# Performance work log

Measured on AMD Instinct MI355X. Metric: run time of the kernel, lower is better.

The kernel has to match this reference:

```python
import math
import jax, jax.numpy as jnp
import numpy as np

B, S, D, H, REL_V = 2, 2048, 1024, 16, 64
HD = D // H
EPS = 1e-5


def _layernorm(x, w, b):
    # torch-style: std with Bessel correction (unbiased), divide by (std + eps)
    u = x.mean(-1, keepdims=True)
    xc = x - u
    s = jnp.sqrt((xc * xc).sum(-1, keepdims=True) / (x.shape[-1] - 1))
    return w * (xc / (s + EPS)) + b


def _gelu(x):
    return 0.5 * x * (1 + jnp.tanh(math.sqrt(2 / math.pi) * (x + 0.044715 * x ** 3)))


def setup_inputs() -> dict:
    key = jax.random.key(0)
    ks = jax.random.split(key, 6)
    wscale = 0.02
    return {
        "x": jax.random.normal(ks[0], (B, S, D), jnp.float32),
        "rel": jax.random.randint(ks[1], (B, S, S), 0, REL_V, jnp.int32),
        "ln1_w": jnp.ones((D,), jnp.float32),
        "ln1_b": jnp.zeros((D,), jnp.float32),
        "Wqkv": jax.random.normal(ks[2], (D, 3 * D), jnp.float32) * wscale,
        "bqkv": jnp.zeros((3 * D,), jnp.float32),
        "Wo": jax.random.normal(ks[3], (D, D), jnp.float32) * wscale,
        "bo": jnp.zeros((D,), jnp.float32),
        "rel_emb": jax.random.normal(ks[4], (REL_V, H), jnp.float32) * wscale,
        "ln2_w": jnp.ones((D,), jnp.float32),
        "ln2_b": jnp.zeros((D,), jnp.float32),
        "Wfc": jax.random.normal(ks[5], (D, 4 * D), jnp.float32) * wscale,
        "bfc": jnp.zeros((4 * D,), jnp.float32),
        "Wp": jax.random.normal(jax.random.fold_in(key, 7), (4 * D, D), jnp.float32) * wscale,
        "bp": jnp.zeros((D,), jnp.float32),
    }


def reference(x, rel, ln1_w, ln1_b, Wqkv, bqkv, Wo, bo, rel_emb,
              ln2_w, ln2_b, Wfc, bfc, Wp, bp):
    h = _layernorm(x, ln1_w, ln1_b)
    qkv = h @ Wqkv + bqkv  # [B,S,3D]
    q, k, v = jnp.split(qkv, 3, axis=-1)
    q = q.reshape(B, S, H, HD).transpose(0, 2, 1, 3)  # [B,H,S,HD]
    k = k.reshape(B, S, H, HD).transpose(0, 2, 1, 3)
    v = v.reshape(B, S, H, HD).transpose(0, 2, 1, 3)

    w = jnp.einsum('bhqd,bhkd->bhqk', q, k) / math.sqrt(HD)  # scale=True
    mask = jnp.tril(jnp.ones((S, S), w.dtype))  # causal tril buffer
    w = w * mask - 1e10 * (1 - mask)
    # faithful to original: rel bias multiplies masked logits (zeroing masked -1e10)
    relw = rel_emb[rel]                    # [B,S,S,H]
    relw = relw.transpose(0, 3, 1, 2)      # [B,H,S,S]
    w = w * (relw * mask)
    p = jax.nn.softmax(w, axis=-1)
    a = jnp.einsum('bhqk,bhkd->bhqd', p, v)       # [B,H,S,HD]
    a = a.transpose(0, 2, 1, 3).reshape(B, S, D)  # merge heads
    a = a @ Wo + bo

    x = x + a
    m = _gelu(_layernorm(x, ln2_w, ln2_b) @ Wfc + bfc) @ Wp + bp
    return x + m
```

## Files before the change

kernel.cpp:

```cpp
#include <hip/hip_runtime.h>
#include <hip/hip_bf16.h>
#include <math.h>

using bf16 = __hip_bfloat16;
typedef __bf16 bf16x8 __attribute__((ext_vector_type(8)));
typedef float f32x4 __attribute__((ext_vector_type(4)));

#define SEQ 2048
#define DIM 1024
#define NH 16
#define HDIM 64
#define BATCH 2

__device__ __forceinline__ void load_lds16(const bf16* g, bf16* l) {
  __builtin_amdgcn_global_load_lds((__attribute__((address_space(1))) void*)g,
                                   (__attribute__((address_space(3))) void*)l, 16, 0, 0);
}

__global__ __launch_bounds__(256) void transpose_k(const float* __restrict__ in,
                                                   bf16* __restrict__ out, int R, int C) {
  __shared__ float tile[32][33];
  int c0 = blockIdx.x * 32, r0 = blockIdx.y * 32;
  int tx = threadIdx.x, ty = threadIdx.y;
#pragma unroll
  for (int j = 0; j < 4; ++j)
    tile[ty + 8 * j][tx] = in[(size_t)(r0 + ty + 8 * j) * C + c0 + tx];
  __syncthreads();
#pragma unroll
  for (int j = 0; j < 4; ++j)
    out[(size_t)(c0 + ty + 8 * j) * R + r0 + tx] = __float2bfloat16(tile[tx][ty + 8 * j]);
}

__global__ __launch_bounds__(256) void ln_k(const float* __restrict__ x,
                                            const float* __restrict__ w,
                                            const float* __restrict__ bb,
                                            bf16* __restrict__ out) {
  int row = blockIdx.x, tid = threadIdx.x;
  int wid = tid >> 6, lane = tid & 63;
  const float* xr = x + (size_t)row * DIM;
  float4 vv = *(const float4*)&xr[tid * 4];
  float v[4] = {vv.x, vv.y, vv.z, vv.w};
  float s = v[0] + v[1] + v[2] + v[3];
#pragma unroll
  for (int m = 1; m < 64; m <<= 1) s += __shfl_xor(s, m, 64);
  __shared__ float red[8];
  if (lane == 0) red[wid] = s;
  __syncthreads();
  float mean = (red[0] + red[1] + red[2] + red[3]) * (1.f / DIM);
  float q = 0.f;
#pragma unroll
  for (int j = 0; j < 4; ++j) {
    v[j] -= mean;
    q += v[j] * v[j];
  }
#pragma unroll
  for (int m = 1; m < 64; m <<= 1) q += __shfl_xor(q, m, 64);
  if (lane == 0) red[4 + wid] = q;
  __syncthreads();
  float ssq = red[4] + red[5] + red[6] + red[7];
  float sd = sqrtf(ssq / (float)(DIM - 1));
  float inv = 1.f / (sd + 1e-5f);
  float4 wv = *(const float4*)&w[tid * 4];
  float4 bv4 = *(const float4*)&bb[tid * 4];
  float wl[4] = {wv.x, wv.y, wv.z, wv.w};
  float bl[4] = {bv4.x, bv4.y, bv4.z, bv4.w};
  unsigned short pk[4];
#pragma unroll
  for (int j = 0; j < 4; ++j)
    pk[j] = __bfloat16_as_ushort(__float2bfloat16(wl[j] * (v[j] * inv) + bl[j]));
  *(uint2*)&out[(size_t)row * DIM + tid * 4] = *(uint2*)pk;
}

__global__ __launch_bounds__(512) void gemm256_k(
    const bf16* __restrict__ A, const bf16* __restrict__ Bt, const float* __restrict__ bias,
    int N, int K, int mode, bf16* __restrict__ o0, bf16* __restrict__ o1,
    bf16* __restrict__ o2) {
  __shared__ bf16 LDSb[65536];
  int tid = threadIdx.x;
  int wid = tid >> 6, lane = tid & 63, quad = lane >> 4, l15 = lane & 15;
  int wm = wid >> 2, wn = wid & 3;
  int m0 = blockIdx.y * 256, n0 = blockIdx.x * 256;
  int grow = lane >> 2;
  int gslot = (lane & 3) ^ ((lane >> 3) & 3);
  const int nt = K >> 6;

  float bv[4];
#pragma unroll
  for (int nf = 0; nf < 4; ++nf) bv[nf] = bias[n0 + wn * 64 + nf * 16 + l15];

  auto stageA = [&](int tile, int ks) {
    int bd = tile & 1;
#pragma unroll
    for (int it = 0; it < 2; ++it) {
      int c = wid * 2 + it;
      load_lds16(A + (size_t)(m0 + c * 16 + grow) * K + tile * 64 + ks * 32 + gslot * 8,
                 &LDSb[bd * 32768 + ks * 8192 + c * 512]);
    }
  };
  auto stageB = [&](int tile, int ks) {
    int bd = tile & 1;
#pragma unroll
    for (int it = 0; it < 2; ++it) {
      int c = wid * 2 + it;
      load_lds16(Bt + (size_t)(n0 + c * 16 + grow) * K + tile * 64 + ks * 32 + gslot * 8,
                 &LDSb[bd * 32768 + 16384 + ks * 8192 + c * 512]);
    }
  };

  f32x4 acc[8][4] = {};
  bf16x8 bq[4];

  stageA(0, 0); stageB(0, 0);
  stageA(0, 1); stageB(0, 1);
  stageA(1, 0); stageB(1, 0);
  asm volatile("s_waitcnt vmcnt(8)" ::: "memory");
  __builtin_amdgcn_sched_barrier(0);
  __builtin_amdgcn_s_barrier();
  __builtin_amdgcn_sched_barrier(0);

#define PHASE(BD, KS, MH, LOADB, STAGE_STMT, WAIT_STMT)                                      \
  {                                                                                          \
    bf16x8 af[4];                                                                            \
    _Pragma("unroll") for (int j = 0; j < 4; ++j) {                                          \
      int r = wm * 128 + (MH) * 64 + j * 16 + l15;                                           \
      af[j] = *(const bf16x8*)&LDSb[(BD) * 32768 + (KS) * 8192 + (r >> 4) * 512 +            \
                                    (r & 15) * 32 + ((quad ^ ((r >> 1) & 3)) << 3)];         \
    }                                                                                        \
    if (LOADB) {                                                                             \
      _Pragma("unroll") for (int n = 0; n < 4; ++n) {                                        \
        int r = wn * 64 + n * 16 + l15;                                                      \
        bq[n] = *(const bf16x8*)&LDSb[(BD) * 32768 + 16384 + (KS) * 8192 + (r >> 4) * 512 +  \
                                      (r & 15) * 32 + ((quad ^ ((r >> 1) & 3)) << 3)];       \
      }                                                                                      \
    }                                                                                        \
    STAGE_STMT;                                                                              \
    __builtin_amdgcn_sched_barrier(0);                                                       \
    __builtin_amdgcn_s_barrier();                                                            \
    __builtin_amdgcn_sched_barrier(0);                                                       \
    __builtin_amdgcn_s_setprio(1);                                                           \
    _Pragma("unroll") for (int j = 0; j < 4; ++j)                                            \
        _Pragma("unroll") for (int n = 0; n < 4; ++n)                                        \
            acc[(MH) * 4 + j][n] = __builtin_amdgcn_mfma_f32_16x16x32_bf16(                  \
                af[j], bq[n], acc[(MH) * 4 + j][n], 0, 0, 0);                                \
    __builtin_amdgcn_s_setprio(0);                                                           \
    WAIT_STMT;                                                                               \
    __builtin_amdgcn_sched_barrier(0);                                                       \
    __builtin_amdgcn_s_barrier();                                                            \
    __builtin_amdgcn_sched_barrier(0);                                                       \
  }

  for (int t = 0; t < nt; ++t) {
    int bd = t & 1;
    PHASE(bd, 0, 0, 1, { if (t + 1 < nt) stageA(t + 1, 1); }, {});
    PHASE(bd, 0, 1, 0, { if (t + 1 < nt) stageB(t + 1, 1); }, {
      if (t + 1 < nt) asm volatile("s_waitcnt vmcnt(8)" ::: "memory");
      else            asm volatile("s_waitcnt vmcnt(0)" ::: "memory");
    });
    PHASE(bd, 1, 0, 1, { if (t + 2 < nt) stageA(t + 2, 0); }, {});
    PHASE(bd, 1, 1, 0, { if (t + 2 < nt) stageB(t + 2, 0); }, {
      if (t + 2 < nt)      asm volatile("s_waitcnt vmcnt(8)" ::: "memory");
      else if (t + 1 < nt) asm volatile("s_waitcnt vmcnt(4)" ::: "memory");
    });
  }
#undef PHASE

#pragma unroll
  for (int mf = 0; mf < 8; ++mf) {
#pragma unroll
    for (int nf = 0; nf < 4; ++nf) {
      int col = n0 + wn * 64 + nf * 16 + l15;
      int row_base = m0 + wm * 128 + mf * 16 + quad * 4;
      if (mode == 0) {
        int which = col >> 10, d = col & 1023, hh = d >> 6, dd = d & 63;
        int b = row_base >> 11, s2 = row_base & 2047;
        if (which == 2) {
          unsigned short pk[4];
#pragma unroll
          for (int r = 0; r < 4; ++r)
            pk[r] = __bfloat16_as_ushort(__float2bfloat16(acc[mf][nf][r] + bv[nf]));
          *(uint2*)&o2[(((size_t)b * NH + hh) * HDIM + dd) * SEQ + s2] = *(uint2*)pk;
        } else {
          bf16* dst = which == 0 ? o0 : o1;
#pragma unroll
          for (int r = 0; r < 4; ++r)
            dst[(((size_t)b * NH + hh) * SEQ + s2 + r) * HDIM + dd] =
                __float2bfloat16(acc[mf][nf][r] + bv[nf]);
        }
      } else {
#pragma unroll
        for (int r = 0; r < 4; ++r) {
          float t2 = acc[mf][nf][r] + bv[nf];
          float u = 0.7978845608028654f * (t2 + 0.044715f * t2 * t2 * t2);
          float g = t2 / (1.f + __expf(-2.f * u));
          o0[(size_t)(row_base + r) * N + col] = __float2bfloat16(g);
        }
      }
    }
  }
}

template <int TM>
__global__ __launch_bounds__(256) void gemm_k(
    const bf16* __restrict__ A, const bf16* __restrict__ Bt, const float* __restrict__ bias,
    int M, int N, int K, int mode,
    const float* __restrict__ residf, float* __restrict__ x2out, const float* __restrict__ x2in,
    float* __restrict__ outf) {
  constexpr int MT = TM / 32;
  constexpr int ACH = TM / 8;
  __shared__ bf16 As[TM * 64];
  __shared__ bf16 Bs[128 * 64];
  int tid = threadIdx.x;
  int wid = tid >> 6, lane = tid & 63, quad = lane >> 4, l15 = lane & 15;
  int wm = wid >> 1, wn = wid & 1;
  int m0 = blockIdx.y * TM, n0 = blockIdx.x * 128;
  int rsub = lane >> 3;
  int c8 = (lane & 7) ^ rsub;
  f32x4 acc[MT][4] = {};

  for (int k0 = 0; k0 < K; k0 += 64) {
    __syncthreads();
#pragma unroll
    for (int it = 0; it < ACH / 4; ++it) {
      int c = wid * (ACH / 4) + it;
      int row = c * 8 + rsub;
      load_lds16(A + (size_t)(m0 + row) * K + k0 + c8 * 8, &As[c * 512]);
    }
#pragma unroll
    for (int it = 0; it < 4; ++it) {
      int c = wid * 4 + it;
      int row = c * 8 + rsub;
      load_lds16(Bt + (size_t)(n0 + row) * K + k0 + c8 * 8, &Bs[c * 512]);
    }
    __syncthreads();
#pragma unroll
    for (int ks = 0; ks < 2; ++ks) {
      bf16x8 af[MT], bfr[4];
#pragma unroll
      for (int mt = 0; mt < MT; ++mt) {
        int r = wm * (MT * 16) + mt * 16 + l15;
        af[mt] = *(const bf16x8*)&As[r * 64 + ((ks * 4 + quad) ^ (r & 7)) * 8];
      }
#pragma unroll
      for (int nt2 = 0; nt2 < 4; ++nt2) {
        int r = wn * 64 + nt2 * 16 + l15;
        bfr[nt2] = *(const bf16x8*)&Bs[r * 64 + ((ks * 4 + quad) ^ (r & 7)) * 8];
      }
#pragma unroll
      for (int mt = 0; mt < MT; ++mt)
#pragma unroll
        for (int nt2 = 0; nt2 < 4; ++nt2)
          acc[mt][nt2] =
              __builtin_amdgcn_mfma_f32_16x16x32_bf16(af[mt], bfr[nt2], acc[mt][nt2], 0, 0, 0);
    }
  }

#pragma unroll
  for (int mt = 0; mt < MT; ++mt) {
#pragma unroll
    for (int nt = 0; nt < 4; ++nt) {
      int col = n0 + wn * 64 + nt * 16 + l15;
      float bvs = bias[col];
      int row_base = m0 + wm * (MT * 16) + mt * 16 + quad * 4;
#pragma unroll
      for (int r = 0; r < 4; ++r) {
        int row = row_base + r;
        float val = acc[mt][nt][r] + bvs;
        size_t i = (size_t)row * N + col;
        if (mode == 1) x2out[i] = residf[i] + val;
        else           outf[i] = x2in[i] + val;
      }
    }
  }
}

__global__ __launch_bounds__(256) void sufv_k(const bf16* __restrict__ vt,
                                              float* __restrict__ suf) {
  int row = blockIdx.x;
  const bf16* src = vt + (size_t)row * SEQ;
  float* dst = suf + (size_t)row * SEQ;
  int tid = threadIdx.x;
  float v[8];
  float s = 0.f;
#pragma unroll
  for (int j = 0; j < 8; ++j) {
    v[j] = __bfloat162float(src[tid * 8 + j]);
    s += v[j];
  }
  __shared__ float sc[256];
  sc[tid] = s;
  __syncthreads();
  for (int off = 1; off < 256; off <<= 1) {
    float add = (tid + off < 256) ? sc[tid + off] : 0.f;
    __syncthreads();
    sc[tid] += add;
    __syncthreads();
  }
  float run = (tid < 255) ? sc[tid + 1] : 0.f;
#pragma unroll
  for (int j = 7; j >= 0; --j) {
    dst[tid * 8 + j] = run;
    run += v[j];
  }
}

__device__ __forceinline__ int pswz(int row) { return (row & 7) ^ (((row >> 3) & 1) << 1); }

__global__ __launch_bounds__(256) void attn_k(const bf16* __restrict__ q,
                                              const bf16* __restrict__ k,
                                              const bf16* __restrict__ v,
                                              const int* __restrict__ rel,
                                              const float* __restrict__ rel_emb,
                                              const float* __restrict__ suf,
                                              bf16* __restrict__ out) {
  int h = blockIdx.x;
  int qt = (SEQ / 64 - 1) - blockIdx.y;
  int b = blockIdx.z;
  int tid = threadIdx.x;
  int wid = tid >> 6, lane = tid & 63, quad = lane >> 4, l15 = lane & 15;

  __shared__ __align__(16) char SM[40960];
  bf16* Kb = (bf16*)SM;
  bf16* Vb = (bf16*)(SM + 16384);
  bf16* Ps = (bf16*)(SM + 32768);
  float(*SufLds)[68] = (float(*)[68])SM;

  const size_t bh = (size_t)b * NH + h;
  const bf16* qb = q + (bh * SEQ + (size_t)qt * 64) * HDIM;
  const bf16* kb0 = k + bh * SEQ * HDIM;
  const bf16* vt0 = v + bh * (size_t)HDIM * SEQ;

  float rv = 0.125f * rel_emb[lane * NH + h];

  int rsub = lane >> 3;
  int c8 = (lane & 7) ^ rsub;

  bf16x8 aq[2];
#pragma unroll
  for (int ks = 0; ks < 2; ++ks)
    aq[ks] = *(const bf16x8*)(qb + (size_t)(wid * 16 + l15) * HDIM + ks * 32 + quad * 8);

#pragma unroll
  for (int it = 0; it < 2; ++it) {
    int c = wid * 2 + it;
    int row = c * 8 + rsub;
    load_lds16(kb0 + (size_t)row * HDIM + c8 * 8, &Kb[c * 512]);
    load_lds16(vt0 + (size_t)row * SEQ + c8 * 8, &Vb[c * 512]);
  }

  const int* relq = rel + (size_t)b * SEQ * SEQ + (size_t)qt * 64 * SEQ;
  const int* rp[4];
#pragma unroll
  for (int r = 0; r < 4; ++r) rp[r] = relq + (size_t)(wid * 16 + quad * 4 + r) * SEQ;

  int ridx[4][4];
#pragma unroll
  for (int nt = 0; nt < 4; ++nt)
#pragma unroll
    for (int r = 0; r < 4; ++r) ridx[nt][r] = rp[r][nt * 16 + l15];

  __syncthreads();

  const int q_base = qt * 64 + wid * 16 + quad * 4;
  const int prow_w = wid * 16 + quad * 4;
  const int prow_r = wid * 16 + l15;
  const int psw_r = pswz(prow_r);
  float l_part[4] = {0.f, 0.f, 0.f, 0.f};
  f32x4 o_acc[4] = {};

  for (int kt = 0; kt < qt; ++kt) {
    int cur = kt & 1;
    int ridx2[4][4];
    {
      bf16* Kd = Kb + (cur ^ 1) * 4096;
      bf16* Vd = Vb + (cur ^ 1) * 4096;
#pragma unroll
      for (int it = 0; it < 2; ++it) {
        int c = wid * 2 + it;
        int row = c * 8 + rsub;
        load_lds16(kb0 + (size_t)((kt + 1) * 64 + row) * HDIM + c8 * 8, &Kd[c * 512]);
        load_lds16(vt0 + (size_t)row * SEQ + (kt + 1) * 64 + c8 * 8, &Vd[c * 512]);
      }
#pragma unroll
      for (int nt = 0; nt < 4; ++nt)
#pragma unroll
        for (int r = 0; r < 4; ++r) ridx2[nt][r] = rp[r][(kt + 1) * 64 + nt * 16 + l15];
    }

    const bf16* Ksb = Kb + cur * 4096;
    const bf16* Vtb = Vb + cur * 4096;

    f32x4 sacc[4] = {};
    __builtin_amdgcn_s_setprio(1);
#pragma unroll
    for (int ks = 0; ks < 2; ++ks) {
#pragma unroll
      for (int nt = 0; nt < 4; ++nt) {
        bf16x8 bfr = *(const bf16x8*)&Ksb[(nt * 16 + l15) * 64 + ((ks * 4 + quad) ^ (l15 & 7)) * 8];
        sacc[nt] = __builtin_amdgcn_mfma_f32_16x16x32_bf16(aq[ks], bfr, sacc[nt], 0, 0, 0);
      }
    }
    __builtin_amdgcn_s_setprio(0);

#pragma unroll
    for (int nt = 0; nt < 4; ++nt) {
#pragma unroll
      for (int r = 0; r < 4; ++r) {
        float m = __shfl(rv, ridx[nt][r], 64);
        float p = __expf(sacc[nt][r] * m);
        l_part[r] += p;
        int row = prow_w + r;
        int sw = (nt * 2 + (l15 >> 3)) ^ pswz(row);
        Ps[row * 64 + sw * 8 + (l15 & 7)] = __float2bfloat16(p);
      }
    }

    __builtin_amdgcn_s_setprio(1);
#pragma unroll
    for (int ks = 0; ks < 2; ++ks) {
      bf16x8 af = *(const bf16x8*)&Ps[prow_r * 64 + ((ks * 4 + quad) ^ psw_r) * 8];
#pragma unroll
      for (int nt = 0; nt < 4; ++nt) {
        bf16x8 bfr = *(const bf16x8*)&Vtb[(nt * 16 + l15) * 64 + ((ks * 4 + quad) ^ (l15 & 7)) * 8];
        o_acc[nt] = __builtin_amdgcn_mfma_f32_16x16x32_bf16(af, bfr, o_acc[nt], 0, 0, 0);
      }
    }
    __builtin_amdgcn_s_setprio(0);

    __syncthreads();

#pragma unroll
    for (int nt = 0; nt < 4; ++nt)
#pragma unroll
      for (int r = 0; r < 4; ++r) ridx[nt][r] = ridx2[nt][r];
  }

  {
    int cur = qt & 1;
    const bf16* Ksb = Kb + cur * 4096;
    const bf16* Vtb = Vb + cur * 4096;

    f32x4 sacc[4] = {};
    __builtin_amdgcn_s_setprio(1);
#pragma unroll
    for (int ks = 0; ks < 2; ++ks) {
#pragma unroll
      for (int nt = 0; nt < 4; ++nt) {
        bf16x8 bfr = *(const bf16x8*)&Ksb[(nt * 16 + l15) * 64 + ((ks * 4 + quad) ^ (l15 & 7)) * 8];
        sacc[nt] = __builtin_amdgcn_mfma_f32_16x16x32_bf16(aq[ks], bfr, sacc[nt], 0, 0, 0);
      }
    }
    __builtin_amdgcn_s_setprio(0);

#pragma unroll
    for (int nt = 0; nt < 4; ++nt) {
#pragma unroll
      for (int r = 0; r < 4; ++r) {
        float m = __shfl(rv, ridx[nt][r], 64);
        float p = __expf(sacc[nt][r] * m);
        int k_abs = qt * 64 + nt * 16 + l15;
        if (k_abs > q_base + r) p = 0.f;
        l_part[r] += p;
        int row = prow_w + r;
        int sw = (nt * 2 + (l15 >> 3)) ^ pswz(row);
        Ps[row * 64 + sw * 8 + (l15 & 7)] = __float2bfloat16(p);
      }
    }

    __builtin_amdgcn_s_setprio(1);
#pragma unroll
    for (int ks = 0; ks < 2; ++ks) {
      bf16x8 af = *(const bf16x8*)&Ps[prow_r * 64 + ((ks * 4 + quad) ^ psw_r) * 8];
#pragma unroll
      for (int nt = 0; nt < 4; ++nt) {
        bf16x8 bfr = *(const bf16x8*)&Vtb[(nt * 16 + l15) * 64 + ((ks * 4 + quad) ^ (l15 & 7)) * 8];
        o_acc[nt] = __builtin_amdgcn_mfma_f32_16x16x32_bf16(af, bfr, o_acc[nt], 0, 0, 0);
      }
    }
    __builtin_amdgcn_s_setprio(0);

    __syncthreads();
  }

#pragma unroll
  for (int r = 0; r < 4; ++r)
#pragma unroll
    for (int m = 1; m < 16; m <<= 1) l_part[r] += __shfl_xor(l_part[r], m, 64);

  const float* sufb = suf + bh * (size_t)HDIM * SEQ + (size_t)qt * 64;
#pragma unroll
  for (int p = 0; p < 4; ++p) {
    int idx = p * 256 + tid;
    int d = idx >> 4, qq = idx & 15;
    *(float4*)&SufLds[d][qq * 4] = *(const float4*)(sufb + (size_t)d * SEQ + qq * 4);
  }
  __syncthreads();

#pragma unroll
  for (int nt = 0; nt < 4; ++nt) {
    int d = nt * 16 + l15;
#pragma unroll
    for (int r = 0; r < 4; ++r) {
      int row = q_base + r;
      int cnt = (SEQ - 1) - row;
      float l = l_part[r] + (float)cnt;
      int q_local = wid * 16 + quad * 4 + r;
      float ov = (o_acc[nt][r] + SufLds[d][q_local]) / l;
      out[((size_t)b * SEQ + row) * DIM + h * HDIM + d] = __float2bfloat16(ov);
    }
  }
}

extern "C" void kernel_launch(void* const* d_in, const int* in_sizes, int n_in,
                              void* d_out, int out_size, void* d_ws, size_t ws_size,
                              hipStream_t stream) {
  const float* x = (const float*)d_in[0];
  const int* rel = (const int*)d_in[1];
  const float* ln1w = (const float*)d_in[2];
  const float* ln1b = (const float*)d_in[3];
  const float* Wqkv = (const float*)d_in[4];
  const float* bqkv = (const float*)d_in[5];
  const float* Wo = (const float*)d_in[6];
  const float* bo = (const float*)d_in[7];
  const float* rel_emb = (const float*)d_in[8];
  const float* ln2w = (const float*)d_in[9];
  const float* ln2b = (const float*)d_in[10];
  const float* Wfc = (const float*)d_in[11];
  const float* bfc = (const float*)d_in[12];
  const float* Wp = (const float*)d_in[13];
  const float* bp = (const float*)d_in[14];
  float* outp = (float*)d_out;

  char* ws = (char*)d_ws;
  const size_t MB = 1u << 20;
  bf16* h = (bf16*)(ws + 0);
  bf16* qb = (bf16*)(ws + 8 * MB);
  bf16* kb = (bf16*)(ws + 16 * MB);
  bf16* vb = (bf16*)(ws + 24 * MB);
  float* x2 = (float*)(ws + 32 * MB);
  float* suf = (float*)(ws + 32 * MB);
  bf16* fcb = (bf16*)(ws + 48 * MB);
  bf16* wqkvT = (bf16*)(ws + 48 * MB);
  bf16* woT = (bf16*)(ws + 54 * MB);
  bf16* wfcT = (bf16*)(ws + 16 * MB);
  bf16* wpT = (bf16*)(ws + 24 * MB);

  dim3 tb(32, 8);
  transpose_k<<<dim3(3072 / 32, 1024 / 32), tb, 0, stream>>>(Wqkv, wqkvT, 1024, 3072);
  transpose_k<<<dim3(1024 / 32, 1024 / 32), tb, 0, stream>>>(Wo, woT, 1024, 1024);

  ln_k<<<BATCH * SEQ, 256, 0, stream>>>(x, ln1w, ln1b, h);

  gemm256_k<<<dim3(3072 / 256, 4096 / 256), 512, 0, stream>>>(
      h, wqkvT, bqkv, 3072, 1024, 0, qb, kb, vb);

  sufv_k<<<BATCH * NH * HDIM, 256, 0, stream>>>(vb, suf);

  attn_k<<<dim3(NH, SEQ / 64, BATCH), 256, 0, stream>>>(qb, kb, vb, rel, rel_emb, suf, h);

  gemm_k<64><<<dim3(1024 / 128, 4096 / 64), 256, 0, stream>>>(
      h, woT, bo, BATCH * SEQ, 1024, 1024, 1, x, x2, nullptr, nullptr);

  transpose_k<<<dim3(4096 / 32, 1024 / 32), tb, 0, stream>>>(Wfc, wfcT, 1024, 4096);
  transpose_k<<<dim3(1024 / 32, 4096 / 32), tb, 0, stream>>>(Wp, wpT, 4096, 1024);

  ln_k<<<BATCH * SEQ, 256, 0, stream>>>(x2, ln2w, ln2b, qb);

  gemm256_k<<<dim3(4096 / 256, 4096 / 256), 512, 0, stream>>>(
      qb, wfcT, bfc, 4096, 1024, 2, fcb, nullptr, nullptr);

  gemm_k<64><<<dim3(1024 / 128, 4096 / 64), 256, 0, stream>>>(
      fcb, wpT, bp, BATCH * SEQ, 1024, 4096, 3, nullptr, nullptr, x2, outp);
}
```

Before: 399.9 us.

## Pair complementary causal query tiles per block to balance attention work

The attention kernel now launches 512-thread blocks, where each block handles two query tiles: tile 31-y and tile y. This pairs long and short causal rows so every block does about the same number of K/V tiles. The two 4-wave groups share one set of K/V tiles loaded into LDS, and the group with the short tile sits idle on the later iterations. This removes the tail imbalance of the causal grid and halves the K/V reloads. The cost is idle waves in the short group, larger LDS per block and fewer blocks.

```diff
diff --git a/kernel.cpp b/kernel.cpp
--- a/kernel.cpp
+++ b/kernel.cpp
@@ -305,7 +305,7 @@
 
 __device__ __forceinline__ int pswz(int row) { return (row & 7) ^ (((row >> 3) & 1) << 1); }
 
-__global__ __launch_bounds__(256) void attn_k(const bf16* __restrict__ q,
+__global__ __launch_bounds__(512) void attn_k(const bf16* __restrict__ q,
                                               const bf16* __restrict__ k,
                                               const bf16* __restrict__ v,
                                               const int* __restrict__ rel,
@@ -313,21 +313,25 @@
                                               const float* __restrict__ suf,
                                               bf16* __restrict__ out) {
   int h = blockIdx.x;
-  int qt = (SEQ / 64 - 1) - blockIdx.y;
+  int y = blockIdx.y;
   int b = blockIdx.z;
   int tid = threadIdx.x;
   int wid = tid >> 6, lane = tid & 63, quad = lane >> 4, l15 = lane & 15;
-
-  __shared__ __align__(16) char SM[40960];
+  int g = wid >> 2;
+  int w4 = wid & 3;
+
+  __shared__ __align__(16) char SM[49152];
   bf16* Kb = (bf16*)SM;
   bf16* Vb = (bf16*)(SM + 16384);
   bf16* Ps = (bf16*)(SM + 32768);
-  float(*SufLds)[68] = (float(*)[68])SM;
+
+  const int qt_hi = 31 - y;
+  const int qtg = g ? y : qt_hi;
 
   const size_t bh = (size_t)b * NH + h;
-  const bf16* qb = q + (bh * SEQ + (size_t)qt * 64) * HDIM;
   const bf16* kb0 = k + bh * SEQ * HDIM;
   const bf16* vt0 = v + bh * (size_t)HDIM * SEQ;
+  const bf16* qb = q + (bh * SEQ + (size_t)qtg * 64) * HDIM;
 
   float rv = 0.125f * rel_emb[lane * NH + h];
 
@@ -337,20 +341,19 @@
   bf16x8 aq[2];
 #pragma unroll
   for (int ks = 0; ks < 2; ++ks)
-    aq[ks] = *(const bf16x8*)(qb + (size_t)(wid * 16 + l15) * HDIM + ks * 32 + quad * 8);
-
-#pragma unroll
-  for (int it = 0; it < 2; ++it) {
-    int c = wid * 2 + it;
+    aq[ks] = *(const bf16x8*)(qb + (size_t)(w4 * 16 + l15) * HDIM + ks * 32 + quad * 8);
+
+  {
+    int c = wid;
     int row = c * 8 + rsub;
     load_lds16(kb0 + (size_t)row * HDIM + c8 * 8, &Kb[c * 512]);
     load_lds16(vt0 + (size_t)row * SEQ + c8 * 8, &Vb[c * 512]);
   }
 
-  const int* relq = rel + (size_t)b * SEQ * SEQ + (size_t)qt * 64 * SEQ;
+  const int* relq = rel + (size_t)b * SEQ * SEQ + (size_t)qtg * 64 * SEQ;
   const int* rp[4];
 #pragma unroll
-  for (int r = 0; r < 4; ++r) rp[r] = relq + (size_t)(wid * 16 + quad * 4 + r) * SEQ;
+  for (int r = 0; r < 4; ++r) rp[r] = relq + (size_t)(w4 * 16 + quad * 4 + r) * SEQ;
 
   int ridx[4][4];
 #pragma unroll
@@ -360,125 +363,102 @@
 
   __syncthreads();
 
-  const int q_base = qt * 64 + wid * 16 + quad * 4;
-  const int prow_w = wid * 16 + quad * 4;
-  const int prow_r = wid * 16 + l15;
+  const int q_base = qtg * 64 + w4 * 16 + quad * 4;
+  const int prow_w = g * 64 + w4 * 16 + quad * 4;
+  const int prow_r = g * 64 + w4 * 16 + l15;
   const int psw_r = pswz(prow_r);
   float l_part[4] = {0.f, 0.f, 0.f, 0.f};
   f32x4 o_acc[4] = {};
 
-  for (int kt = 0; kt < qt; ++kt) {
+  for (int kt = 0; kt <= qt_hi; ++kt) {
     int cur = kt & 1;
-    int ridx2[4][4];
-    {
+
+    if (kt < qt_hi) {
       bf16* Kd = Kb + (cur ^ 1) * 4096;
       bf16* Vd = Vb + (cur ^ 1) * 4096;
-#pragma unroll
-      for (int it = 0; it < 2; ++it) {
-        int c = wid * 2 + it;
-        int row = c * 8 + rsub;
-        load_lds16(kb0 + (size_t)((kt + 1) * 64 + row) * HDIM + c8 * 8, &Kd[c * 512]);
-        load_lds16(vt0 + (size_t)row * SEQ + (kt + 1) * 64 + c8 * 8, &Vd[c * 512]);
-      }
+      int c = wid;
+      int row = c * 8 + rsub;
+      load_lds16(kb0 + (size_t)((kt + 1) * 64 + row) * HDIM + c8 * 8, &Kd[c * 512]);
+      load_lds16(vt0 + (size_t)row * SEQ + (kt + 1) * 64 + c8 * 8, &Vd[c * 512]);
+    }
+    int ridx2[4][4];
+    bool nxt_active = (kt < qt_hi) && (kt + 1 <= qtg);
+    if (nxt_active) {
 #pragma unroll
       for (int nt = 0; nt < 4; ++nt)
 #pragma unroll
         for (int r = 0; r < 4; ++r) ridx2[nt][r] = rp[r][(kt + 1) * 64 + nt * 16 + l15];
     }
 
-    const bf16* Ksb = Kb + cur * 4096;
-    const bf16* Vtb = Vb + cur * 4096;
-
-    f32x4 sacc[4] = {};
-    __builtin_amdgcn_s_setprio(1);
-#pragma unroll
-    for (int ks = 0; ks < 2; ++ks) {
-#pragma unroll
-      for (int nt = 0; nt < 4; ++nt) {
-        bf16x8 bfr = *(const bf16x8*)&Ksb[(nt * 16 + l15) * 64 + ((ks * 4 + quad) ^ (l15 & 7)) * 8];
-        sacc[nt] = __builtin_amdgcn_mfma_f32_16x16x32_bf16(aq[ks], bfr, sacc[nt], 0, 0, 0);
-      }
-    }
-    __builtin_amdgcn_s_setprio(0);
-
-#pragma unroll
-    for (int nt = 0; nt < 4; ++nt) {
-#pragma unroll
-      for (int r = 0; r < 4; ++r) {
-        float m = __shfl(rv, ridx[nt][r], 64);
-        float p = __expf(sacc[nt][r] * m);
-        l_part[r] += p;
-        int row = prow_w + r;
-        int sw = (nt * 2 + (l15 >> 3)) ^ pswz(row);
-        Ps[row * 64 + sw * 8 + (l15 & 7)] = __float2bfloat16(p);
-      }
-    }
-
-    __builtin_amdgcn_s_setprio(1);
-#pragma unroll
-    for (int ks = 0; ks < 2; ++ks) {
-      bf16x8 af = *(const bf16x8*)&Ps[prow_r * 64 + ((ks * 4 + quad) ^ psw_r) * 8];
-#pragma unroll
-      for (int nt = 0; nt < 4; ++nt) {
-        bf16x8 bfr = *(const bf16x8*)&Vtb[(nt * 16 + l15) * 64 + ((ks * 4 + quad) ^ (l15 & 7)) * 8];
-        o_acc[nt] = __builtin_amdgcn_mfma_f32_16x16x32_bf16(af, bfr, o_acc[nt], 0, 0, 0);
-      }
-    }
-    __builtin_amdgcn_s_setprio(0);
+    if (kt <= qtg) {
+      const bf16* Ksb = Kb + cur * 4096;
+      const bf16* Vtb = Vb + cur * 4096;
+
+      f32x4 sacc[4] = {};
+      __builtin_amdgcn_s_setprio(1);
+#pragma unroll
+      for (int ks = 0; ks < 2; ++ks) {
+#pragma unroll
+        for (int nt = 0; nt < 4; ++nt) {
+          bf16x8 bfr =
+              *(const bf16x8*)&Ksb[(nt * 16 + l15) * 64 + ((ks * 4 + quad) ^ (l15 & 7)) * 8];
+          sacc[nt] = __builtin_amdgcn_mfma_f32_16x16x32_bf16(aq[ks], bfr, sacc[nt], 0, 0, 0);
+        }
+      }
+      __builtin_amdgcn_s_setprio(0);
+
+      if (kt == qtg) {
+#pragma unroll
+        for (int nt = 0; nt < 4; ++nt) {
+#pragma unroll
+          for (int r = 0; r < 4; ++r) {
+            float m = __shfl(rv, ridx[nt][r], 64);
+            float p = __expf(sacc[nt][r] * m);
+            int k_abs = kt * 64 + nt * 16 + l15;
+            if (k_abs > q_base + r) p = 0.f;
+            l_part[r] += p;
+            int row = prow_w + r;
+            int sw = (nt * 2 + (l15 >> 3)) ^ pswz(row);
+            Ps[row * 64 + sw * 8 + (l15 & 7)] = __float2bfloat16(p);
+          }
+        }
+      } else {
+#pragma unroll
+        for (int nt = 0; nt < 4; ++nt) {
+#pragma unroll
+          for (int r = 0; r < 4; ++r) {
+            float m = __shfl(rv, ridx[nt][r], 64);
+            float p = __expf(sacc[nt][r] * m);
+            l_part[r] += p;
+            int row = prow_w + r;
+            int sw = (nt * 2 + (l15 >> 3)) ^ pswz(row);
+            Ps[row * 64 + sw * 8 + (l15 & 7)] = __float2bfloat16(p);
+          }
+        }
+      }
+
+      __builtin_amdgcn_s_setprio(1);
+#pragma unroll
+      for (int ks = 0; ks < 2; ++ks) {
+        bf16x8 af = *(const bf16x8*)&Ps[prow_r * 64 + ((ks * 4 + quad) ^ psw_r) * 8];
+#pragma unroll
+        for (int nt = 0; nt < 4; ++nt) {
+          bf16x8 bfr =
+              *(const bf16x8*)&Vtb[(nt * 16 + l15) * 64 + ((ks * 4 + quad) ^ (l15 & 7)) * 8];
+          o_acc[nt] = __builtin_amdgcn_mfma_f32_16x16x32_bf16(af, bfr, o_acc[nt], 0, 0, 0);
+        }
+      }
+      __builtin_amdgcn_s_setprio(0);
+    }
 
     __syncthreads();
 
-#pragma unroll
-    for (int nt = 0; nt < 4; ++nt)
-#pragma unroll
-      for (int r = 0; r < 4; ++r) ridx[nt][r] = ridx2[nt][r];
-  }
-
-  {
-    int cur = qt & 1;
-    const bf16* Ksb = Kb + cur * 4096;
-    const bf16* Vtb = Vb + cur * 4096;
-
-    f32x4 sacc[4] = {};
-    __builtin_amdgcn_s_setprio(1);
-#pragma unroll
-    for (int ks = 0; ks < 2; ++ks) {
-#pragma unroll
-      for (int nt = 0; nt < 4; ++nt) {
-        bf16x8 bfr = *(const bf16x8*)&Ksb[(nt * 16 + l15) * 64 + ((ks * 4 + quad) ^ (l15 & 7)) * 8];
-        sacc[nt] = __builtin_amdgcn_mfma_f32_16x16x32_bf16(aq[ks], bfr, sacc[nt], 0, 0, 0);
-      }
-    }
-    __builtin_amdgcn_s_setprio(0);
-
-#pragma unroll
-    for (int nt = 0; nt < 4; ++nt) {
-#pragma unroll
-      for (int r = 0; r < 4; ++r) {
-        float m = __shfl(rv, ridx[nt][r], 64);
-        float p = __expf(sacc[nt][r] * m);
-        int k_abs = qt * 64 + nt * 16 + l15;
-        if (k_abs > q_base + r) p = 0.f;
-        l_part[r] += p;
-        int row = prow_w + r;
-        int sw = (nt * 2 + (l15 >> 3)) ^ pswz(row);
-        Ps[row * 64 + sw * 8 + (l15 & 7)] = __float2bfloat16(p);
-      }
-    }
-
-    __builtin_amdgcn_s_setprio(1);
-#pragma unroll
-    for (int ks = 0; ks < 2; ++ks) {
-      bf16x8 af = *(const bf16x8*)&Ps[prow_r * 64 + ((ks * 4 + quad) ^ psw_r) * 8];
-#pragma unroll
-      for (int nt = 0; nt < 4; ++nt) {
-        bf16x8 bfr = *(const bf16x8*)&Vtb[(nt * 16 + l15) * 64 + ((ks * 4 + quad) ^ (l15 & 7)) * 8];
-        o_acc[nt] = __builtin_amdgcn_mfma_f32_16x16x32_bf16(af, bfr, o_acc[nt], 0, 0, 0);
-      }
-    }
-    __builtin_amdgcn_s_setprio(0);
-
-    __syncthreads();
+    if (nxt_active) {
+#pragma unroll
+      for (int nt = 0; nt < 4; ++nt)
+#pragma unroll
+        for (int r = 0; r < 4; ++r) ridx[nt][r] = ridx2[nt][r];
+    }
   }
 
 #pragma unroll
@@ -486,10 +466,12 @@
 #pragma unroll
     for (int m = 1; m < 16; m <<= 1) l_part[r] += __shfl_xor(l_part[r], m, 64);
 
-  const float* sufb = suf + bh * (size_t)HDIM * SEQ + (size_t)qt * 64;
+  float(*SufLds)[68] = (float(*)[68])(SM + g * 17408);
+  const float* sufb = suf + bh * (size_t)HDIM * SEQ + (size_t)qtg * 64;
+  int tg = tid & 255;
 #pragma unroll
   for (int p = 0; p < 4; ++p) {
-    int idx = p * 256 + tid;
+    int idx = p * 256 + tg;
     int d = idx >> 4, qq = idx & 15;
     *(float4*)&SufLds[d][qq * 4] = *(const float4*)(sufb + (size_t)d * SEQ + qq * 4);
   }
@@ -503,7 +485,7 @@
       int row = q_base + r;
       int cnt = (SEQ - 1) - row;
       float l = l_part[r] + (float)cnt;
-      int q_local = wid * 16 + quad * 4 + r;
+      int q_local = w4 * 16 + quad * 4 + r;
       float ov = (o_acc[nt][r] + SufLds[d][q_local]) / l;
       out[((size_t)b * SEQ + row) * DIM + h * HDIM + d] = __float2bfloat16(ov);
     }
@@ -555,7 +537,7 @@
 
   sufv_k<<<BATCH * NH * HDIM, 256, 0, stream>>>(vb, suf);
 
-  attn_k<<<dim3(NH, SEQ / 64, BATCH), 256, 0, stream>>>(qb, kb, vb, rel, rel_emb, suf, h);
+  attn_k<<<dim3(NH, 16, BATCH), 512, 0, stream>>>(qb, kb, vb, rel, rel_emb, suf, h);
 
   gemm_k<64><<<dim3(1024 / 128, 4096 / 64), 256, 0, stream>>>(
       h, woT, bo, BATCH * SEQ, 1024, 1024, 1, x, x2, nullptr, nullptr);
```

Result: slower. 434.1 us (+8.6%).
